# Optimization experiments

Hardware: AMD Instinct MI355X
Metric: run time of the kernel (lower is better)

Reference implementation:

```python
import jax, jax.numpy as jnp
import numpy as np

BN_EPS = 1e-5


def setup_inputs() -> dict:
    key = jax.random.key(0)
    ks = jax.random.split(key, 13)
    B, C, H, W = 8, 256, 96, 32
    D = C // 2  # inter_channels
    s = 0.05
    return {
        "x": jax.random.normal(ks[0], (B, C, H, W), jnp.float32),
        "g_w": jax.random.normal(ks[1], (D, C), jnp.float32) * s,
        "g_b": jax.random.normal(ks[2], (D,), jnp.float32) * s,
        "theta_w": jax.random.normal(ks[3], (D, C), jnp.float32) * s,
        "theta_b": jax.random.normal(ks[4], (D,), jnp.float32) * s,
        "phi_w": jax.random.normal(ks[5], (D, C), jnp.float32) * s,
        "phi_b": jax.random.normal(ks[6], (D,), jnp.float32) * s,
        "w_w": jax.random.normal(ks[7], (C, D), jnp.float32) * s,
        "w_b": jax.random.normal(ks[8], (C,), jnp.float32) * s,
        "bn_gamma": jax.random.normal(ks[9], (C,), jnp.float32),
        "bn_beta": jax.random.normal(ks[10], (C,), jnp.float32) * s,
        "bn_mean": jax.random.normal(ks[11], (C,), jnp.float32) * s,
        "bn_var": jax.random.uniform(ks[12], (C,), jnp.float32),
    }


def reference(x, g_w, g_b, theta_w, theta_b, phi_w, phi_b, w_w, w_b,
              bn_gamma, bn_beta, bn_mean, bn_var):
    B, C, H, W = x.shape
    N = H * W
    xf = x.reshape(B, C, N)  # flatten spatial: (B, C, N)

    # 1x1 conv projections == per-pixel linear maps
    g_x = jnp.einsum('dc,bcn->bnd', g_w, xf) + g_b            # (B, N, D)
    theta_x = jnp.einsum('dc,bcn->bnd', theta_w, xf) + theta_b  # (B, N, D)
    phi_x = jnp.einsum('dc,bcn->bdn', phi_w, xf) + phi_b[:, None]  # (B, D, N)

    # unnormalized attention: f = theta phi^T / N, then y = f g
    f_div_C = jnp.einsum('bnd,bdm->bnm', theta_x, phi_x) / N  # (B, N, N)
    y = jnp.einsum('bnm,bmd->bnd', f_div_C, g_x)              # (B, N, D)

    # output 1x1 conv + eval-mode BatchNorm2d
    wy = jnp.einsum('cd,bnd->bcn', w_w, y) + w_b[:, None]     # (B, C, N)
    inv = bn_gamma / jnp.sqrt(bn_var + BN_EPS)
    wy = (wy - bn_mean[:, None]) * inv[:, None] + bn_beta[:, None]

    z = wy.reshape(B, C, H, W) + x  # residual
    return z
```

## Files before the change

kernel.cpp:

```cpp
#include <hip/hip_runtime.h>
#include <hip/hip_bf16.h>
#include <cstddef>

typedef __attribute__((ext_vector_type(8))) short short8;
typedef __attribute__((ext_vector_type(4))) short short4v;
typedef __attribute__((ext_vector_type(4))) float floatx4;
typedef __hip_bfloat16 bf16;

#define NB 8
#define NC 256
#define ND 128
#define NN 3072
#define NBLK 48
#define BN_EPS 1e-5f

static __device__ __forceinline__ short f2s(float v) {
    bf16 h = __float2bfloat16(v);
    return *reinterpret_cast<short*>(&h);
}

__global__ __launch_bounds__(256) void setup_kernel(
    const float* __restrict__ phi_w, const float* __restrict__ g_w,
    const float* __restrict__ theta_w, short* __restrict__ Wall)
{
    int t = threadIdx.x;
    int r = blockIdx.x;
    const float* src = (r < 128) ? (phi_w + (size_t)r * NC)
                     : (r < 256) ? (g_w + (size_t)(r - 128) * NC)
                                 : (theta_w + (size_t)(r - 256) * NC);
    Wall[(size_t)r * NC + t] = f2s(src[t]);
}

__global__ __launch_bounds__(384)
void proj_kernel(const float* __restrict__ x, const short* __restrict__ Wall,
                 const float* __restrict__ phi_b, const float* __restrict__ g_b,
                 const float* __restrict__ theta_b,
                 short* __restrict__ thDN, float* __restrict__ Mpart)
{
    __shared__ short PGs[256][72];
    __shared__ short Xs[64][72];
    int b = blockIdx.y;
    int n0 = blockIdx.x * 64;
    int t = threadIdx.x;
    int lane = t & 63;
    int wave = t >> 6;
    int lm = lane & 15;
    int lk = (lane >> 4) * 8;

    const float* xb = x + (size_t)b * NC * NN;

    floatx4 zero = {0.f, 0.f, 0.f, 0.f};
    floatx4 acc[4][4];
#pragma unroll
    for (int i = 0; i < 4; ++i)
#pragma unroll
        for (int j = 0; j < 4; ++j) acc[i][j] = zero;

    int sn = t & 63, cg = t >> 6;
    const float* srcp = xb + (size_t)(cg * 16) * NN + n0 + sn;
    float xf[16];
    if (t < 256) {
#pragma unroll
        for (int j = 0; j < 16; ++j) xf[j] = srcp[(size_t)j * NN];
    }

#pragma unroll
    for (int kt = 0; kt < NC; kt += 64) {
        __syncthreads();
        short8 af2[2][4];
#pragma unroll
        for (int h = 0; h < 2; ++h)
#pragma unroll
            for (int i = 0; i < 4; ++i)
                af2[h][i] = *(const short8*)(Wall +
                        (size_t)(wave * 64 + i * 16 + lm) * NC + kt + h * 32 + lk);
        if (t < 256) {
            short8 s0, s1;
#pragma unroll
            for (int j = 0; j < 8; ++j) {
                s0[j] = f2s(xf[j]);
                s1[j] = f2s(xf[8 + j]);
            }
            *(short8*)&Xs[sn][cg * 16]     = s0;
            *(short8*)&Xs[sn][cg * 16 + 8] = s1;
        }
        __syncthreads();
        if (t < 256 && kt < NC - 64) {
            const float* np = srcp + (size_t)(kt + 64) * NN;
#pragma unroll
            for (int j = 0; j < 16; ++j) xf[j] = np[(size_t)j * NN];
        }
#pragma unroll
        for (int h = 0; h < 2; ++h) {
            int kk = h * 32;
            short8 bfr[4];
#pragma unroll
            for (int j = 0; j < 4; ++j)
                bfr[j] = *(const short8*)&Xs[j * 16 + lm][kk + lk];
#pragma unroll
            for (int i = 0; i < 4; ++i)
#pragma unroll
                for (int j = 0; j < 4; ++j)
                    acc[i][j] = __builtin_amdgcn_mfma_f32_16x16x32_bf16(
                        af2[h][i], bfr[j], acc[i][j], 0, 0, 0);
        }
    }

    int row0 = wave * 64 + (lane >> 4) * 4;

    if (wave < 4) {
#pragma unroll
        for (int i = 0; i < 4; ++i) {
#pragma unroll
            for (int r = 0; r < 4; ++r) {
                int row = row0 + i * 16 + r;
                float bv = (row < 128) ? phi_b[row] : g_b[row - 128];
#pragma unroll
                for (int j = 0; j < 4; ++j)
                    PGs[row][lm + j * 16] = f2s(acc[i][j][r] + bv);
            }
        }
    } else {
        short* Tb = thDN + (size_t)b * ND * NN;
#pragma unroll
        for (int i = 0; i < 4; ++i) {
#pragma unroll
            for (int r = 0; r < 4; ++r) {
                int d = row0 - 256 + i * 16 + r;
                float bv = theta_b[d];
#pragma unroll
                for (int j = 0; j < 4; ++j)
                    Tb[(size_t)d * NN + n0 + lm + j * 16] =
                        f2s(acc[i][j][r] + bv);
            }
        }
    }
    __syncthreads();

    if (wave < 4) {
        int wr = wave >> 1, wc = wave & 1;
        floatx4 macc[4][4];
#pragma unroll
        for (int i = 0; i < 4; ++i)
#pragma unroll
            for (int j = 0; j < 4; ++j) macc[i][j] = zero;
#pragma unroll
        for (int kk = 0; kk < 64; kk += 32) {
            short8 af[4], bfr[4];
#pragma unroll
            for (int i = 0; i < 4; ++i)
                af[i] = *(const short8*)&PGs[wr * 64 + i * 16 + lm][kk + lk];
#pragma unroll
            for (int j = 0; j < 4; ++j)
                bfr[j] = *(const short8*)&PGs[128 + wc * 64 + j * 16 + lm][kk + lk];
#pragma unroll
            for (int i = 0; i < 4; ++i)
#pragma unroll
                for (int j = 0; j < 4; ++j)
                    macc[i][j] = __builtin_amdgcn_mfma_f32_16x16x32_bf16(
                        af[i], bfr[j], macc[i][j], 0, 0, 0);
        }
        float* Mf = Mpart + ((size_t)b * NBLK + blockIdx.x) * (ND * ND);
        int mr0 = wr * 64 + (lane >> 4) * 4;
        int mc0 = wc * 64 + lm;
        const float sc = 1.f / (float)NN;
#pragma unroll
        for (int i = 0; i < 4; ++i)
#pragma unroll
            for (int j = 0; j < 4; ++j)
#pragma unroll
                for (int r = 0; r < 4; ++r)
                    Mf[(size_t)(mr0 + i * 16 + r) * ND + mc0 + j * 16] =
                        macc[i][j][r] * sc;
    }
}

__global__ __launch_bounds__(256)
void reduce_kernel(const float* __restrict__ Mpart, short* __restrict__ Mb16)
{
    int idx4 = (blockIdx.x * 256 + threadIdx.x) * 4;
    const float* src = Mpart + (size_t)(idx4 >> 14) * (NBLK * 16384)
                             + (idx4 & 16383);
    floatx4 s = {0.f, 0.f, 0.f, 0.f};
#pragma unroll 12
    for (int p = 0; p < NBLK; ++p)
        s += *(const floatx4*)(src + (size_t)p * 16384);
    short4v o;
#pragma unroll
    for (int j = 0; j < 4; ++j) o[j] = f2s(s[j]);
    *(short4v*)(Mb16 + idx4) = o;
}

__global__ __launch_bounds__(256)
void final_kernel(const short* __restrict__ Mb16, const short* __restrict__ thDN,
                  const float* __restrict__ w_w, const float* __restrict__ w_b,
                  const float* __restrict__ gamma, const float* __restrict__ beta,
                  const float* __restrict__ mean, const float* __restrict__ var,
                  const float* __restrict__ x, float* __restrict__ out)
{
    __shared__ short As[128][72];
    __shared__ short Bs[128][72];
    __shared__ short P2s[128][136];
    int b = blockIdx.z;
    int tile_m = blockIdx.y * 128;
    int tile_n = blockIdx.x * 128;
    int t = threadIdx.x;
    int lane = t & 63;
    int wave = t >> 6;
    int wr = wave >> 1, wc = wave & 1;
    int lm = lane & 15;
    int lk = (lane >> 4) * 8;
    int ch = (t & 7) * 8;
    int r0 = t >> 3;
    int dl = t & 63;
    int ng = t >> 6;

    const short* Mb = Mb16 + (size_t)b * ND * ND;
    const short* Tb = thDN + (size_t)b * ND * NN;
    const short* tsrc = Tb + (size_t)dl * NN + tile_n + ng * 32;

    floatx4 zero = {0.f, 0.f, 0.f, 0.f};
    floatx4 acc[4][4];
#pragma unroll
    for (int i = 0; i < 4; ++i)
#pragma unroll
        for (int j = 0; j < 4; ++j) acc[i][j] = zero;

    floatx4 av0[4], av1[4];
    short8 bv[4];
#pragma unroll
    for (int p = 0; p < 4; ++p) {
        int r = r0 + p * 32;
        const float* ap = w_w + (size_t)(tile_m + r) * ND + ch;
        av0[p] = *(const floatx4*)ap;
        av1[p] = *(const floatx4*)(ap + 4);
        bv[p]  = *(const short8*)(Mb + (size_t)r * ND + ch);
    }
    short8 tv[4];

#pragma unroll
    for (int kt = 0; kt < ND; kt += 64) {
        __syncthreads();
#pragma unroll
        for (int p = 0; p < 4; ++p) {
            int r = r0 + p * 32;
            short8 sa;
#pragma unroll
            for (int j = 0; j < 4; ++j) {
                sa[j]     = f2s(av0[p][j]);
                sa[4 + j] = f2s(av1[p][j]);
            }
            *(short8*)&As[r][ch] = sa;
            *(short8*)&Bs[r][ch] = bv[p];
        }
        __syncthreads();
        if (kt == 0) {
#pragma unroll
            for (int p = 0; p < 4; ++p) {
                int r = r0 + p * 32;
                const float* ap = w_w + (size_t)(tile_m + r) * ND + 64 + ch;
                av0[p] = *(const floatx4*)ap;
                av1[p] = *(const floatx4*)(ap + 4);
                bv[p]  = *(const short8*)(Mb + (size_t)r * ND + 64 + ch);
            }
        } else {
#pragma unroll
            for (int q = 0; q < 4; ++q)
                tv[q] = *(const short8*)(tsrc + q * 8);
        }
#pragma unroll
        for (int kk = 0; kk < 64; kk += 32) {
            short8 af[4], bfr[4];
#pragma unroll
            for (int i = 0; i < 4; ++i)
                af[i] = *(const short8*)&As[wr * 64 + i * 16 + lm][kk + lk];
#pragma unroll
            for (int j = 0; j < 4; ++j)
                bfr[j] = *(const short8*)&Bs[wc * 64 + j * 16 + lm][kk + lk];
#pragma unroll
            for (int i = 0; i < 4; ++i)
#pragma unroll
                for (int j = 0; j < 4; ++j)
                    acc[i][j] = __builtin_amdgcn_mfma_f32_16x16x32_bf16(
                        af[i], bfr[j], acc[i][j], 0, 0, 0);
        }
    }

    {
        int row0 = wr * 64 + (lane >> 4) * 4;
        int col0 = wc * 64 + lm;
#pragma unroll
        for (int i = 0; i < 4; ++i) {
#pragma unroll
            for (int r = 0; r < 4; ++r) {
                int cl = row0 + i * 16 + r;
                int c = tile_m + cl;
                float iv = gamma[c] * rsqrtf(var[c] + BN_EPS);
#pragma unroll
                for (int j = 0; j < 4; ++j)
                    P2s[cl][col0 + j * 16] = f2s(acc[i][j][r] * iv);
            }
        }
    }

    floatx4 acc2[4][4];
#pragma unroll
    for (int i = 0; i < 4; ++i)
#pragma unroll
        for (int j = 0; j < 4; ++j) acc2[i][j] = zero;

#pragma unroll
    for (int kt = 0; kt < ND; kt += 64) {
        __syncthreads();
#pragma unroll
        for (int q = 0; q < 4; ++q)
#pragma unroll
            for (int jj = 0; jj < 8; ++jj)
                Bs[ng * 32 + q * 8 + jj][dl] = tv[q][jj];
        __syncthreads();
        if (kt == 0) {
#pragma unroll
            for (int q = 0; q < 4; ++q)
                tv[q] = *(const short8*)(tsrc + (size_t)64 * NN + q * 8);
        }
#pragma unroll
        for (int kk = 0; kk < 64; kk += 32) {
            short8 af[4], bfr[4];
#pragma unroll
            for (int i = 0; i < 4; ++i)
                af[i] = *(const short8*)&P2s[wr * 64 + i * 16 + lm][kt + kk + lk];
#pragma unroll
            for (int j = 0; j < 4; ++j)
                bfr[j] = *(const short8*)&Bs[wc * 64 + j * 16 + lm][kk + lk];
#pragma unroll
            for (int i = 0; i < 4; ++i)
#pragma unroll
                for (int j = 0; j < 4; ++j)
                    acc2[i][j] = __builtin_amdgcn_mfma_f32_16x16x32_bf16(
                        af[i], bfr[j], acc2[i][j], 0, 0, 0);
        }
    }

    int crow0 = tile_m + wr * 64 + (lane >> 4) * 4;
    int col0 = tile_n + wc * 64 + lm;
    float* Cf = out + (size_t)b * NC * NN;
    const float* Rg = x + (size_t)b * NC * NN;
#pragma unroll
    for (int i = 0; i < 4; ++i) {
#pragma unroll
        for (int r = 0; r < 4; ++r) {
            int c = crow0 + i * 16 + r;
            float iv = gamma[c] * rsqrtf(var[c] + BN_EPS);
            float b2 = iv * (w_b[c] - mean[c]) + beta[c];
#pragma unroll
            for (int j = 0; j < 4; ++j) {
                size_t idx = (size_t)c * NN + col0 + j * 16;
                Cf[idx] = acc2[i][j][r] + b2 + Rg[idx];
            }
        }
    }
}

extern "C" void kernel_launch(void* const* d_in, const int* in_sizes, int n_in,
                              void* d_out, int out_size, void* d_ws, size_t ws_size,
                              hipStream_t stream)
{
    const float* x       = (const float*)d_in[0];
    const float* g_w     = (const float*)d_in[1];
    const float* g_b     = (const float*)d_in[2];
    const float* theta_w = (const float*)d_in[3];
    const float* theta_b = (const float*)d_in[4];
    const float* phi_w   = (const float*)d_in[5];
    const float* phi_b   = (const float*)d_in[6];
    const float* w_w     = (const float*)d_in[7];
    const float* w_b     = (const float*)d_in[8];
    const float* gamma   = (const float*)d_in[9];
    const float* beta    = (const float*)d_in[10];
    const float* mean    = (const float*)d_in[11];
    const float* var     = (const float*)d_in[12];
    (void)in_sizes; (void)n_in; (void)out_size; (void)ws_size;

    char* w = (char*)d_ws;
    short* thDN  = (short*)w; w += (size_t)NB * ND * NN * 2;
    float* Mpart = (float*)w; w += (size_t)NB * NBLK * ND * ND * 4;
    short* Mb16  = (short*)w; w += (size_t)NB * ND * ND * 2;
    short* Wall  = (short*)w; w += (size_t)384 * NC * 2;

    setup_kernel<<<dim3(384), dim3(256), 0, stream>>>(
        phi_w, g_w, theta_w, Wall);

    proj_kernel<<<dim3(NN / 64, NB), dim3(384), 0, stream>>>(
        x, Wall, phi_b, g_b, theta_b, thDN, Mpart);

    reduce_kernel<<<dim3(128), dim3(256), 0, stream>>>(Mpart, Mb16);

    final_kernel<<<dim3(NN / 128, NC / 128, NB), 256, 0, stream>>>(
        Mb16, thDN, w_w, w_b, gamma, beta, mean, var, x, (float*)d_out);
}
```

Baseline: 133.6 us.

## Precompute W·M product per batch in reduce kernel; shrink final kernel tiles

```diff
diff --git a/kernel.cpp b/kernel.cpp
--- a/kernel.cpp
+++ b/kernel.cpp
@@ -176,173 +176,157 @@
 }
 
 __global__ __launch_bounds__(256)
-void reduce_kernel(const float* __restrict__ Mpart, short* __restrict__ Mb16)
-{
-    int idx4 = (blockIdx.x * 256 + threadIdx.x) * 4;
-    const float* src = Mpart + (size_t)(idx4 >> 14) * (NBLK * 16384)
-                             + (idx4 & 16383);
-    floatx4 s = {0.f, 0.f, 0.f, 0.f};
+void reduce_p2_kernel(const float* __restrict__ Mpart,
+                      const float* __restrict__ w_w,
+                      const float* __restrict__ gamma,
+                      const float* __restrict__ var,
+                      short* __restrict__ P2g)
+{
+    __shared__ short As[256][136];
+    __shared__ short Ms[16][136];
+    int blk = blockIdx.x;
+    int b = blk >> 4;
+    int e0 = (blk & 15) * 8;
+    int t = threadIdx.x;
+    int lane = t & 63;
+    int wave = t >> 6;
+    int lm = lane & 15;
+    int lk = (lane >> 4) * 8;
+
+    {
+        short4v z = {0, 0, 0, 0};
+        *(short4v*)&Ms[8 + (t >> 5)][(t & 31) * 4] = z;
+    }
+
+    {
+        int fo = t * 4;
+        int e = fo >> 7;
+        int d = fo & 127;
+        const float* src = Mpart + (size_t)b * (NBLK * 16384) + (size_t)e0 * 128 + fo;
+        floatx4 s = {0.f, 0.f, 0.f, 0.f};
 #pragma unroll 12
-    for (int p = 0; p < NBLK; ++p)
-        s += *(const floatx4*)(src + (size_t)p * 16384);
-    short4v o;
-#pragma unroll
-    for (int j = 0; j < 4; ++j) o[j] = f2s(s[j]);
-    *(short4v*)(Mb16 + idx4) = o;
+        for (int p = 0; p < NBLK; ++p)
+            s += *(const floatx4*)(src + (size_t)p * 16384);
+        short4v o;
+#pragma unroll
+        for (int j = 0; j < 4; ++j) o[j] = f2s(s[j]);
+        *(short4v*)&Ms[e][d] = o;
+    }
+
+#pragma unroll
+    for (int p = 0; p < 32; ++p) {
+        int fidx = p * 256 + t;
+        int c = fidx >> 5;
+        int d4 = (fidx & 31) * 4;
+        floatx4 v = *(const floatx4*)(w_w + (size_t)fidx * 4);
+        short4v o;
+#pragma unroll
+        for (int j = 0; j < 4; ++j) o[j] = f2s(v[j]);
+        *(short4v*)&As[c][d4] = o;
+    }
+    __syncthreads();
+
+    floatx4 zero = {0.f, 0.f, 0.f, 0.f};
+    floatx4 acc[4];
+#pragma unroll
+    for (int i = 0; i < 4; ++i) acc[i] = zero;
+#pragma unroll
+    for (int kk = 0; kk < 128; kk += 32) {
+        short8 bfr = *(const short8*)&Ms[lm][kk + lk];
+#pragma unroll
+        for (int i = 0; i < 4; ++i) {
+            short8 af = *(const short8*)&As[wave * 64 + i * 16 + lm][kk + lk];
+            acc[i] = __builtin_amdgcn_mfma_f32_16x16x32_bf16(
+                af, bfr, acc[i], 0, 0, 0);
+        }
+    }
+    if (lm < 8) {
+        int e = e0 + lm;
+#pragma unroll
+        for (int i = 0; i < 4; ++i) {
+#pragma unroll
+            for (int r = 0; r < 4; ++r) {
+                int c = wave * 64 + i * 16 + (lane >> 4) * 4 + r;
+                float iv = gamma[c] * rsqrtf(var[c] + BN_EPS);
+                P2g[((size_t)b * NC + c) * ND + e] = f2s(acc[i][r] * iv);
+            }
+        }
+    }
 }
 
 __global__ __launch_bounds__(256)
-void final_kernel(const short* __restrict__ Mb16, const short* __restrict__ thDN,
-                  const float* __restrict__ w_w, const float* __restrict__ w_b,
+void final_kernel(const short* __restrict__ P2g, const short* __restrict__ thDN,
+                  const float* __restrict__ w_b,
                   const float* __restrict__ gamma, const float* __restrict__ beta,
                   const float* __restrict__ mean, const float* __restrict__ var,
                   const float* __restrict__ x, float* __restrict__ out)
 {
-    __shared__ short As[128][72];
-    __shared__ short Bs[128][72];
-    __shared__ short P2s[128][136];
+    __shared__ short Bs[96][72];
     int b = blockIdx.z;
     int tile_m = blockIdx.y * 128;
-    int tile_n = blockIdx.x * 128;
+    int tile_n = blockIdx.x * 96;
     int t = threadIdx.x;
     int lane = t & 63;
     int wave = t >> 6;
     int wr = wave >> 1, wc = wave & 1;
     int lm = lane & 15;
     int lk = (lane >> 4) * 8;
-    int ch = (t & 7) * 8;
-    int r0 = t >> 3;
     int dl = t & 63;
     int ng = t >> 6;
 
-    const short* Mb = Mb16 + (size_t)b * ND * ND;
+    const short* P2b = P2g + (size_t)b * NC * ND;
     const short* Tb = thDN + (size_t)b * ND * NN;
-    const short* tsrc = Tb + (size_t)dl * NN + tile_n + ng * 32;
+    const short* tsrc = Tb + (size_t)dl * NN + tile_n + ng * 24;
 
     floatx4 zero = {0.f, 0.f, 0.f, 0.f};
-    floatx4 acc[4][4];
+    floatx4 acc2[4][3];
 #pragma unroll
     for (int i = 0; i < 4; ++i)
 #pragma unroll
-        for (int j = 0; j < 4; ++j) acc[i][j] = zero;
-
-    floatx4 av0[4], av1[4];
-    short8 bv[4];
-#pragma unroll
-    for (int p = 0; p < 4; ++p) {
-        int r = r0 + p * 32;
-        const float* ap = w_w + (size_t)(tile_m + r) * ND + ch;
-        av0[p] = *(const floatx4*)ap;
-        av1[p] = *(const floatx4*)(ap + 4);
-        bv[p]  = *(const short8*)(Mb + (size_t)r * ND + ch);
-    }
-    short8 tv[4];
+        for (int j = 0; j < 3; ++j) acc2[i][j] = zero;
+
+    short8 tv[3];
+#pragma unroll
+    for (int q = 0; q < 3; ++q) tv[q] = *(const short8*)(tsrc + q * 8);
 
 #pragma unroll
     for (int kt = 0; kt < ND; kt += 64) {
         __syncthreads();
 #pragma unroll
-        for (int p = 0; p < 4; ++p) {
-            int r = r0 + p * 32;
-            short8 sa;
-#pragma unroll
-            for (int j = 0; j < 4; ++j) {
-                sa[j]     = f2s(av0[p][j]);
-                sa[4 + j] = f2s(av1[p][j]);
-            }
-            *(short8*)&As[r][ch] = sa;
-            *(short8*)&Bs[r][ch] = bv[p];
-        }
+        for (int q = 0; q < 3; ++q)
+#pragma unroll
+            for (int jj = 0; jj < 8; ++jj)
+                Bs[ng * 24 + q * 8 + jj][dl] = tv[q][jj];
         __syncthreads();
+        short8 af2[2][4];
+#pragma unroll
+        for (int h = 0; h < 2; ++h)
+#pragma unroll
+            for (int i = 0; i < 4; ++i)
+                af2[h][i] = *(const short8*)(P2b +
+                    (size_t)(tile_m + wr * 64 + i * 16 + lm) * ND + kt + h * 32 + lk);
         if (kt == 0) {
 #pragma unroll
-            for (int p = 0; p < 4; ++p) {
-                int r = r0 + p * 32;
-                const float* ap = w_w + (size_t)(tile_m + r) * ND + 64 + ch;
-                av0[p] = *(const floatx4*)ap;
-                av1[p] = *(const floatx4*)(ap + 4);
-                bv[p]  = *(const short8*)(Mb + (size_t)r * ND + 64 + ch);
-            }
-        } else {
-#pragma unroll
-            for (int q = 0; q < 4; ++q)
-                tv[q] = *(const short8*)(tsrc + q * 8);
-        }
-#pragma unroll
-        for (int kk = 0; kk < 64; kk += 32) {
-            short8 af[4], bfr[4];
-#pragma unroll
-            for (int i = 0; i < 4; ++i)
-                af[i] = *(const short8*)&As[wr * 64 + i * 16 + lm][kk + lk];
-#pragma unroll
-            for (int j = 0; j < 4; ++j)
-                bfr[j] = *(const short8*)&Bs[wc * 64 + j * 16 + lm][kk + lk];
-#pragma unroll
-            for (int i = 0; i < 4; ++i)
-#pragma unroll
-                for (int j = 0; j < 4; ++j)
-                    acc[i][j] = __builtin_amdgcn_mfma_f32_16x16x32_bf16(
-                        af[i], bfr[j], acc[i][j], 0, 0, 0);
-        }
-    }
-
-    {
-        int row0 = wr * 64 + (lane >> 4) * 4;
-        int col0 = wc * 64 + lm;
-#pragma unroll
-        for (int i = 0; i < 4; ++i) {
-#pragma unroll
-            for (int r = 0; r < 4; ++r) {
-                int cl = row0 + i * 16 + r;
-                int c = tile_m + cl;
-                float iv = gamma[c] * rsqrtf(var[c] + BN_EPS);
-#pragma unroll
-                for (int j = 0; j < 4; ++j)
-                    P2s[cl][col0 + j * 16] = f2s(acc[i][j][r] * iv);
-            }
-        }
-    }
-
-    floatx4 acc2[4][4];
-#pragma unroll
-    for (int i = 0; i < 4; ++i)
-#pragma unroll
-        for (int j = 0; j < 4; ++j) acc2[i][j] = zero;
-
-#pragma unroll
-    for (int kt = 0; kt < ND; kt += 64) {
-        __syncthreads();
-#pragma unroll
-        for (int q = 0; q < 4; ++q)
-#pragma unroll
-            for (int jj = 0; jj < 8; ++jj)
-                Bs[ng * 32 + q * 8 + jj][dl] = tv[q][jj];
-        __syncthreads();
-        if (kt == 0) {
-#pragma unroll
-            for (int q = 0; q < 4; ++q)
+            for (int q = 0; q < 3; ++q)
                 tv[q] = *(const short8*)(tsrc + (size_t)64 * NN + q * 8);
         }
 #pragma unroll
-        for (int kk = 0; kk < 64; kk += 32) {
-            short8 af[4], bfr[4];
-#pragma unroll
-            for (int i = 0; i < 4; ++i)
-                af[i] = *(const short8*)&P2s[wr * 64 + i * 16 + lm][kt + kk + lk];
-#pragma unroll
-            for (int j = 0; j < 4; ++j)
-                bfr[j] = *(const short8*)&Bs[wc * 64 + j * 16 + lm][kk + lk];
-#pragma unroll
-            for (int i = 0; i < 4; ++i)
-#pragma unroll
-                for (int j = 0; j < 4; ++j)
+        for (int h = 0; h < 2; ++h) {
+            short8 bfr[3];
+#pragma unroll
+            for (int j = 0; j < 3; ++j)
+                bfr[j] = *(const short8*)&Bs[wc * 48 + j * 16 + lm][h * 32 + lk];
+#pragma unroll
+            for (int i = 0; i < 4; ++i)
+#pragma unroll
+                for (int j = 0; j < 3; ++j)
                     acc2[i][j] = __builtin_amdgcn_mfma_f32_16x16x32_bf16(
-                        af[i], bfr[j], acc2[i][j], 0, 0, 0);
+                        af2[h][i], bfr[j], acc2[i][j], 0, 0, 0);
         }
     }
 
     int crow0 = tile_m + wr * 64 + (lane >> 4) * 4;
-    int col0 = tile_n + wc * 64 + lm;
+    int col0 = tile_n + wc * 48 + lm;
     float* Cf = out + (size_t)b * NC * NN;
     const float* Rg = x + (size_t)b * NC * NN;
 #pragma unroll
@@ -353,7 +337,7 @@
             float iv = gamma[c] * rsqrtf(var[c] + BN_EPS);
             float b2 = iv * (w_b[c] - mean[c]) + beta[c];
 #pragma unroll
-            for (int j = 0; j < 4; ++j) {
+            for (int j = 0; j < 3; ++j) {
                 size_t idx = (size_t)c * NN + col0 + j * 16;
                 Cf[idx] = acc2[i][j][r] + b2 + Rg[idx];
             }
@@ -383,7 +367,7 @@
     char* w = (char*)d_ws;
     short* thDN  = (short*)w; w += (size_t)NB * ND * NN * 2;
     float* Mpart = (float*)w; w += (size_t)NB * NBLK * ND * ND * 4;
-    short* Mb16  = (short*)w; w += (size_t)NB * ND * ND * 2;
+    short* P2g   = (short*)w; w += (size_t)NB * NC * ND * 2;
     short* Wall  = (short*)w; w += (size_t)384 * NC * 2;
 
     setup_kernel<<<dim3(384), dim3(256), 0, stream>>>(
@@ -392,8 +376,9 @@
     proj_kernel<<<dim3(NN / 64, NB), dim3(384), 0, stream>>>(
         x, Wall, phi_b, g_b, theta_b, thDN, Mpart);
 
-    reduce_kernel<<<dim3(128), dim3(256), 0, stream>>>(Mpart, Mb16);
-
-    final_kernel<<<dim3(NN / 128, NC / 128, NB), 256, 0, stream>>>(
-        Mb16, thDN, w_w, w_b, gamma, beta, mean, var, x, (float*)d_out);
-}
+    reduce_p2_kernel<<<dim3(128), dim3(256), 0, stream>>>(
+        Mpart, w_w, gamma, var, P2g);
+
+    final_kernel<<<dim3(NN / 96, NC / 128, NB), 256, 0, stream>>>(
+        P2g, thDN, w_b, gamma, beta, mean, var, x, (float*)d_out);
+}
```

New measurement: 136.7 us. 2.4% more time.
